# Kernel optimization log

Hardware: AMD Instinct MI355X
Metric: run time of the kernel (lower is better)

Reference implementation:

```python
import jax, jax.numpy as jnp
import numpy as np

# Mamba hyperparameters (match init_kwargs)
D_MODEL = 1024
D_STATE = 16
D_CONV = 4
EXPAND = 2
D_INNER = EXPAND * D_MODEL          # 2048
DT_RANK = D_MODEL // 16             # 64 (ceil(d_model/16))
B, L = 2, 2048
LN_EPS = 1e-5


def setup_inputs() -> dict:
    key = jax.random.key(0)
    ks = jax.random.split(key, 8)
    s = lambda k, shape, scale=0.02: jax.random.normal(k, shape, jnp.float32) * scale
    x = jax.random.normal(ks[0], (B, L, D_MODEL), jnp.float32)
    W_in = s(ks[1], (2 * D_INNER, D_MODEL))                 # in_proj (no bias)
    W_conv = s(ks[2], (D_INNER, 1, D_CONV), 0.1)            # depthwise conv1d weight
    b_conv = jnp.zeros((D_INNER,), jnp.float32)
    W_xproj = s(ks[3], (DT_RANK + 2 * D_STATE, D_INNER))    # x_proj (no bias)
    W_dt = s(ks[4], (D_INNER, DT_RANK), 0.1)                # dt_proj weight
    b_dt = s(ks[5], (D_INNER,), 0.5)                        # dt_proj bias
    # A initialized as -exp(A_log) with A_log = log(1..d_state), as in mamba_ssm
    A_log = jnp.log(jnp.broadcast_to(
        jnp.arange(1, D_STATE + 1, dtype=jnp.float32), (D_INNER, D_STATE)))
    D_skip = jnp.ones((D_INNER,), jnp.float32)
    W_out = s(ks[6], (D_MODEL, D_INNER))                    # out_proj (no bias)
    gamma = jnp.ones((D_MODEL,), jnp.float32)
    beta = jnp.zeros((D_MODEL,), jnp.float32)
    return dict(x=x, W_in=W_in, W_conv=W_conv, b_conv=b_conv, W_xproj=W_xproj,
                W_dt=W_dt, b_dt=b_dt, A_log=A_log, D_skip=D_skip, W_out=W_out,
                gamma=gamma, beta=beta)


def _mamba(x, W_in, W_conv, b_conv, W_xproj, W_dt, b_dt, A_log, D_skip, W_out):
    # in_proj -> split into x branch and gate z branch, each [B, L, d_inner]
    xz = jnp.einsum('bld,ed->ble', x, W_in)
    xin, z = jnp.split(xz, 2, axis=-1)

    # causal depthwise conv1d over time, then SiLU
    xc = jnp.swapaxes(xin, 1, 2)                            # [B, d_inner, L]
    xc = jnp.pad(xc, ((0, 0), (0, 0), (D_CONV - 1, 0)))
    xc = jax.lax.conv_general_dilated(
        xc, W_conv, window_strides=(1,), padding='VALID',
        dimension_numbers=('NCH', 'OIH', 'NCH'), feature_group_count=D_INNER)
    xc = xc + b_conv[None, :, None]
    u = jax.nn.silu(jnp.swapaxes(xc, 1, 2))                 # [B, L, d_inner]

    # input-dependent dt, B, C
    xdb = jnp.einsum('ble,fe->blf', u, W_xproj)
    dt, Bm, Cm = jnp.split(xdb, [DT_RANK, DT_RANK + D_STATE], axis=-1)
    delta = jax.nn.softplus(jnp.einsum('blr,er->ble', dt, W_dt) + b_dt)  # [B,L,E]
    A = -jnp.exp(A_log)                                     # [E, N]

    def step(h, inp):
        d_t, B_t, C_t, u_t = inp                            # [B,E],[B,N],[B,N],[B,E]
        dA = jnp.exp(d_t[..., None] * A)                    # [B, E, N]
        dBu = d_t[..., None] * B_t[:, None, :] * u_t[..., None]
        h = dA * h + dBu                                    # [B, E, N]
        y = jnp.einsum('ben,bn->be', h, C_t)
        return h, y

    h0 = jnp.zeros((B, D_INNER, D_STATE), x.dtype)
    xs = (jnp.swapaxes(delta, 0, 1), jnp.swapaxes(Bm, 0, 1),
          jnp.swapaxes(Cm, 0, 1), jnp.swapaxes(u, 0, 1))
    _, ys = jax.lax.scan(step, h0, xs)                      # ys: [L, B, E]
    y = jnp.swapaxes(ys, 0, 1) + u * D_skip
    y = y * jax.nn.silu(z)                                  # gated
    return jnp.einsum('ble,de->bld', y, W_out)


def reference(x, W_in, W_conv, b_conv, W_xproj, W_dt, b_dt, A_log, D_skip,
              W_out, gamma, beta):
    out = x + _mamba(x, W_in, W_conv, b_conv, W_xproj, W_dt, b_dt, A_log,
                     D_skip, W_out)
    mu = jnp.mean(out, axis=-1, keepdims=True)
    var = jnp.mean(jnp.square(out - mu), axis=-1, keepdims=True)
    return (out - mu) * jax.lax.rsqrt(var + LN_EPS) * gamma + beta
```

## Files before the change

### kernel.cpp

```cpp
#include <hip/hip_runtime.h>
#include <cstdint>
#include <cstddef>

#define D_MODEL   1024
#define D_STATE   16
#define D_CONV    4
#define D_INNER   2048
#define DT_RANK   64
#define NBATCH    2
#define SEQ       2048
#define NTOK      (NBATCH*SEQ)
#define LN_EPSF   1e-5f
#define NCHUNK    64
#define TCHUNK    32
#define KSPLIT    8

typedef unsigned short u16;
typedef __bf16 bf16x8 __attribute__((ext_vector_type(8)));
typedef float  f32x4  __attribute__((ext_vector_type(4)));

__device__ __forceinline__ u16 f2bf(float f) {
  unsigned u = __float_as_uint(f);
  u += 0x7fffu + ((u >> 16) & 1u);
  return (u16)(u >> 16);
}
__device__ __forceinline__ float bf2f(u16 v) {
  return __uint_as_float(((unsigned)v) << 16);
}
__device__ __forceinline__ void unpack8(uint4 v, float* f) {
  f[0] = __uint_as_float(v.x << 16); f[1] = __uint_as_float(v.x & 0xffff0000u);
  f[2] = __uint_as_float(v.y << 16); f[3] = __uint_as_float(v.y & 0xffff0000u);
  f[4] = __uint_as_float(v.z << 16); f[5] = __uint_as_float(v.z & 0xffff0000u);
  f[6] = __uint_as_float(v.w << 16); f[7] = __uint_as_float(v.w & 0xffff0000u);
}

__device__ __forceinline__ void async16(const u16* g, u16* l) {
  __builtin_amdgcn_global_load_lds(
      (const __attribute__((address_space(1))) unsigned*)g,
      (__attribute__((address_space(3))) unsigned*)l, 16, 0, 0);
}

#define PN0 (NTOK*D_MODEL)
#define PN1 (2*D_INNER*D_MODEL)
#define PN2 (128*D_INNER)
#define PN3 (D_INNER*DT_RANK)
#define PN4 (D_MODEL*D_INNER)
#define PTOT (PN0+PN1+PN2+PN3+PN4)
__global__ __launch_bounds__(256) void prep_k(
    const float* __restrict__ x, const float* __restrict__ W_in,
    const float* __restrict__ W_xproj, const float* __restrict__ W_dt,
    const float* __restrict__ W_out,
    u16* __restrict__ x_bf, u16* __restrict__ Win_bf, u16* __restrict__ Wxp_bf,
    u16* __restrict__ Wdt_bf, u16* __restrict__ Wout_bf)
{
  int i = (blockIdx.x * 256 + threadIdx.x) * 4;
  const float* src; u16* dst; bool pad = false; int local = i;
  if (local < PN0)            { src = x;       dst = x_bf; }
  else if ((local -= PN0) < PN1) { src = W_in;    dst = Win_bf; }
  else if ((local -= PN1) < PN2) { src = W_xproj; dst = Wxp_bf; pad = (local >> 11) >= 96; }
  else if ((local -= PN2) < PN3) { src = W_dt;    dst = Wdt_bf; }
  else if ((local -= PN3) < PN4) { src = W_out;   dst = Wout_bf; }
  else return;
  ushort4 o;
  if (pad) { o = (ushort4){0,0,0,0}; }
  else {
    const float4 v = *(const float4*)(src + local);
    o = (ushort4){ f2bf(v.x), f2bf(v.y), f2bf(v.z), f2bf(v.w) };
  }
  *(ushort4*)(dst + local) = o;
}

template<int BM, int BN, int KB, int WTM, int WTN, int EPI>
__global__ __launch_bounds__(256) void gemm_nt(
    const u16* __restrict__ A, const u16* __restrict__ B,
    float* __restrict__ C, u16* __restrict__ Cb,
    const float* __restrict__ bias, const float* __restrict__ res,
    int kStart, int kEnd, int lda, int ldb, int ldc, size_t partStride)
{
  constexpr int CPR  = KB / 8;
  constexpr int MASK = CPR - 1;
  constexpr int KSUB = KB / 32;
  constexpr int WAVES_N = BN / (16 * WTN);
  constexpr int ACH = BM * CPR;
  constexpr int BCH = BN * CPR;
  constexpr int ROUNDS = (ACH + BCH) / 256;

  __shared__ __align__(16) u16 lA[BM * KB];
  __shared__ __align__(16) u16 lB[BN * KB];

  const int tid  = threadIdx.x;
  const int w    = tid >> 6;
  const int lane = tid & 63;
  const int lrow = lane & 15;
  const int quad = lane >> 4;
  const int bm = blockIdx.y * BM;
  const int bn = blockIdx.x * BN;
  const int wave_m = (w / WAVES_N) * (16 * WTM);
  const int wave_n = (w % WAVES_N) * (16 * WTN);

  int kOff = 0;
  if constexpr (EPI == 4) kOff = blockIdx.z * (kEnd - kStart);

  f32x4 acc[WTM][WTN];
  #pragma unroll
  for (int mi = 0; mi < WTM; ++mi)
    #pragma unroll
    for (int ni = 0; ni < WTN; ++ni)
      acc[mi][ni] = (f32x4){0.f, 0.f, 0.f, 0.f};

  for (int k0 = kStart + kOff; k0 < kEnd + kOff; k0 += KB) {
    #pragma unroll
    for (int r = 0; r < ROUNDS; ++r) {
      const int c0 = r * 256 + w * 64;
      const int c  = c0 + lane;
      if (c0 < ACH) {
        const int row = c / CPR, cc = (c & MASK) ^ (row & MASK);
        async16(A + (size_t)(bm + row) * lda + k0 + cc * 8, &lA[c0 * 8]);
      } else {
        const int cb = c - ACH, c0b = c0 - ACH;
        const int row = cb / CPR, cc = (cb & MASK) ^ (row & MASK);
        async16(B + (size_t)(bn + row) * ldb + k0 + cc * 8, &lB[c0b * 8]);
      }
    }
    __syncthreads();

    #pragma unroll
    for (int s = 0; s < KSUB; ++s) {
      bf16x8 af[WTM], bfv[WTN];
      #pragma unroll
      for (int mi = 0; mi < WTM; ++mi) {
        const int R = wave_m + mi * 16 + lrow;
        af[mi] = *(const bf16x8*)&lA[R * KB + (((s * 4 + quad) ^ (R & MASK)) * 8)];
      }
      #pragma unroll
      for (int ni = 0; ni < WTN; ++ni) {
        const int R = wave_n + ni * 16 + lrow;
        bfv[ni] = *(const bf16x8*)&lB[R * KB + (((s * 4 + quad) ^ (R & MASK)) * 8)];
      }
      #pragma unroll
      for (int mi = 0; mi < WTM; ++mi)
        #pragma unroll
        for (int ni = 0; ni < WTN; ++ni)
          acc[mi][ni] = __builtin_amdgcn_mfma_f32_16x16x32_bf16(af[mi], bfv[ni], acc[mi][ni], 0, 0, 0);
    }
    __syncthreads();
  }

  #pragma unroll
  for (int mi = 0; mi < WTM; ++mi) {
    #pragma unroll
    for (int ni = 0; ni < WTN; ++ni) {
      const int col  = bn + wave_n + ni * 16 + lrow;
      const int row0 = bm + wave_m + mi * 16 + quad * 4;
      #pragma unroll
      for (int r = 0; r < 4; ++r) {
        float v = acc[mi][ni][r];
        const size_t idx = (size_t)(row0 + r) * ldc + col;
        if constexpr (EPI == 0) {
          C[idx] = v;
        } else if constexpr (EPI == 1) {
          Cb[idx] = f2bf(v);
        } else if constexpr (EPI == 2) {
          v += bias[col];
          v = (v > 20.f) ? v : log1pf(__expf(v));
          Cb[idx] = f2bf(v);
        } else if constexpr (EPI == 3) {
          C[idx] = v + res[idx];
        } else {
          C[(size_t)blockIdx.z * partStride + idx] = v;
        }
      }
    }
  }
}

__global__ __launch_bounds__(256) void reduce_conv_k(
    const float* __restrict__ part, u16* __restrict__ dst)
{
  const int i = blockIdx.x * 256 + threadIdx.x;
  float s = 0.f;
  #pragma unroll
  for (int p = 0; p < KSPLIT; ++p)
    s += part[(size_t)p * (NTOK * 128) + i];
  dst[i] = f2bf(s);
}

#define CONV_T 8
__global__ __launch_bounds__(256) void conv_silu_k(
    const u16* __restrict__ xz, const float* __restrict__ Wc,
    const float* __restrict__ bc, u16* __restrict__ ub)
{
  const int tid = blockIdx.x * 256 + threadIdx.x;
  const int e   = (tid & 511) * 4;
  const int tb  = tid >> 9;
  const int tok0 = tb * CONV_T;
  const int l0   = tok0 & (SEQ - 1);

  float4 wq[4];
  #pragma unroll
  for (int q = 0; q < 4; ++q) wq[q] = *(const float4*)(Wc + (e + q) * 4);
  const float4 bcv = *(const float4*)(bc + e);

  float p3[4], p2[4], p1[4];
  if (l0 == 0) {
    #pragma unroll
    for (int q = 0; q < 4; ++q) { p3[q] = 0.f; p2[q] = 0.f; p1[q] = 0.f; }
  } else {
    const ushort4 a = *(const ushort4*)(xz + (size_t)(tok0 - 3) * (2 * D_INNER) + e);
    const ushort4 b = *(const ushort4*)(xz + (size_t)(tok0 - 2) * (2 * D_INNER) + e);
    const ushort4 c = *(const ushort4*)(xz + (size_t)(tok0 - 1) * (2 * D_INNER) + e);
    p3[0]=bf2f(a.x); p3[1]=bf2f(a.y); p3[2]=bf2f(a.z); p3[3]=bf2f(a.w);
    p2[0]=bf2f(b.x); p2[1]=bf2f(b.y); p2[2]=bf2f(b.z); p2[3]=bf2f(b.w);
    p1[0]=bf2f(c.x); p1[1]=bf2f(c.y); p1[2]=bf2f(c.z); p1[3]=bf2f(c.w);
  }

  #pragma unroll
  for (int tt = 0; tt < CONV_T; ++tt) {
    const ushort4 xv = *(const ushort4*)(xz + (size_t)(tok0 + tt) * (2 * D_INNER) + e);
    float cur[4] = { bf2f(xv.x), bf2f(xv.y), bf2f(xv.z), bf2f(xv.w) };
    ushort4 o;
    u16* op = (u16*)&o;
    float a0 = ((const float*)&bcv)[0] + p3[0]*wq[0].x + p2[0]*wq[0].y + p1[0]*wq[0].z + cur[0]*wq[0].w;
    float a1 = ((const float*)&bcv)[1] + p3[1]*wq[1].x + p2[1]*wq[1].y + p1[1]*wq[1].z + cur[1]*wq[1].w;
    float a2 = ((const float*)&bcv)[2] + p3[2]*wq[2].x + p2[2]*wq[2].y + p1[2]*wq[2].z + cur[2]*wq[2].w;
    float a3 = ((const float*)&bcv)[3] + p3[3]*wq[3].x + p2[3]*wq[3].y + p1[3]*wq[3].z + cur[3]*wq[3].w;
    op[0] = f2bf(a0 / (1.f + __expf(-a0)));
    op[1] = f2bf(a1 / (1.f + __expf(-a1)));
    op[2] = f2bf(a2 / (1.f + __expf(-a2)));
    op[3] = f2bf(a3 / (1.f + __expf(-a3)));
    *(ushort4*)(ub + (size_t)(tok0 + tt) * D_INNER + e) = o;
    #pragma unroll
    for (int q = 0; q < 4; ++q) { p3[q] = p2[q]; p2[q] = p1[q]; p1[q] = cur[q]; }
  }
}


__global__ __launch_bounds__(256) void scan_p1(
    const u16* __restrict__ delta, const u16* __restrict__ ub,
    const u16* __restrict__ xdb, const float* __restrict__ A_log,
    float* __restrict__ S, float* __restrict__ sumd)
{
  const int e = blockIdx.x * 256 + threadIdx.x;
  const int c = blockIdx.y;
  const int b = blockIdx.z;
  float A[16], h[16];
  bool fast = true;
  #pragma unroll
  for (int n = 0; n < 16; ++n) {
    A[n] = -__expf(A_log[e * 16 + n]);
    fast = fast && (fabsf(A[n] + (float)(n + 1)) < 1e-3f);
    h[n] = 0.f;
  }
  float sd = 0.f;
  const int t0 = c * TCHUNK;
  #pragma unroll 2
  for (int t = 0; t < TCHUNK; ++t) {
    const size_t g = (size_t)(b * SEQ + t0 + t);
    const float dlt = bf2f(delta[g * D_INNER + e]);
    const float ut  = bf2f(ub[g * D_INNER + e]);
    float Bv[16];
    const u16* bp = xdb + g * 128 + DT_RANK;
    unpack8(*(const uint4*)bp, Bv);
    unpack8(*(const uint4*)(bp + 8), Bv + 8);
    sd += dlt;
    const float dbu = dlt * ut;
    float dA[16];
    if (fast) {
      const float q = __expf(-dlt);
      float p = 1.f;
      #pragma unroll
      for (int n = 0; n < 16; ++n) { p *= q; dA[n] = p; }
    } else {
      #pragma unroll
      for (int n = 0; n < 16; ++n) dA[n] = __expf(dlt * A[n]);
    }
    #pragma unroll
    for (int n = 0; n < 16; ++n)
      h[n] = dA[n] * h[n] + dbu * Bv[n];
  }
  const size_t idx = ((size_t)(b * NCHUNK + c) * D_INNER + e);
  #pragma unroll
  for (int q = 0; q < 4; ++q)
    *(f32x4*)&S[idx * 16 + q * 4] = (f32x4){h[q*4], h[q*4+1], h[q*4+2], h[q*4+3]};
  sumd[idx] = sd;
}

__global__ __launch_bounds__(256) void scan_p2(
    const float* __restrict__ S, const float* __restrict__ sumd,
    const float* __restrict__ A_log, float* __restrict__ hinit)
{
  const int tid = blockIdx.x * 256 + threadIdx.x;
  const int n = tid & 15;
  const int e = (tid >> 4) & (D_INNER - 1);
  const int b = tid >> 15;
  const float An = -__expf(A_log[e * 16 + n]);
  float h = 0.f;
  size_t idx = (size_t)b * NCHUNK * D_INNER + e;
  float s_cur  = S[idx * 16 + n];
  float sd_cur = sumd[idx];
  for (int c = 0; c < NCHUNK; ++c) {
    hinit[idx * 16 + n] = h;
    float s_nxt = 0.f, sd_nxt = 0.f;
    if (c + 1 < NCHUNK) {
      const size_t idx2 = idx + D_INNER;
      s_nxt  = S[idx2 * 16 + n];
      sd_nxt = sumd[idx2];
    }
    h = __expf(An * sd_cur) * h + s_cur;
    s_cur = s_nxt; sd_cur = sd_nxt;
    idx += D_INNER;
  }
}

__global__ __launch_bounds__(256) void scan_p3(
    const u16* __restrict__ delta, const u16* __restrict__ ub,
    const u16* __restrict__ xdb, const u16* __restrict__ xz,
    const float* __restrict__ A_log, const float* __restrict__ D_skip,
    const float* __restrict__ hinit, u16* __restrict__ yg)
{
  const int e = blockIdx.x * 256 + threadIdx.x;
  const int c = blockIdx.y;
  const int b = blockIdx.z;
  const size_t idx = ((size_t)(b * NCHUNK + c) * D_INNER + e);
  float A[16], h[16];
  bool fast = true;
  #pragma unroll
  for (int n = 0; n < 16; ++n) {
    A[n] = -__expf(A_log[e * 16 + n]);
    fast = fast && (fabsf(A[n] + (float)(n + 1)) < 1e-3f);
  }
  #pragma unroll
  for (int q = 0; q < 4; ++q) {
    f32x4 v = *(const f32x4*)&hinit[idx * 16 + q * 4];
    h[q*4] = v[0]; h[q*4+1] = v[1]; h[q*4+2] = v[2]; h[q*4+3] = v[3];
  }
  const float De = D_skip[e];
  const int t0 = c * TCHUNK;
  #pragma unroll 2
  for (int t = 0; t < TCHUNK; ++t) {
    const size_t g = (size_t)(b * SEQ + t0 + t);
    const float dlt = bf2f(delta[g * D_INNER + e]);
    const float ut  = bf2f(ub[g * D_INNER + e]);
    const float z   = bf2f(xz[g * (2 * D_INNER) + D_INNER + e]);
    float Bv[16], Cv[16];
    const u16* bp = xdb + g * 128 + DT_RANK;
    unpack8(*(const uint4*)bp, Bv);
    unpack8(*(const uint4*)(bp + 8), Bv + 8);
    unpack8(*(const uint4*)(bp + 16), Cv);
    unpack8(*(const uint4*)(bp + 24), Cv + 8);
    const float dbu = dlt * ut;
    float dA[16];
    if (fast) {
      const float q = __expf(-dlt);
      float p = 1.f;
      #pragma unroll
      for (int n = 0; n < 16; ++n) { p *= q; dA[n] = p; }
    } else {
      #pragma unroll
      for (int n = 0; n < 16; ++n) dA[n] = __expf(dlt * A[n]);
    }
    float y = 0.f;
    #pragma unroll
    for (int n = 0; n < 16; ++n) {
      h[n] = dA[n] * h[n] + dbu * Bv[n];
      y += h[n] * Cv[n];
    }
    y += ut * De;
    const float gt = z / (1.f + __expf(-z));
    yg[g * D_INNER + e] = f2bf(y * gt);
  }
}

__global__ __launch_bounds__(256) void ln_k(const float* __restrict__ pre,
                                            const float* __restrict__ gamma,
                                            const float* __restrict__ beta,
                                            float* __restrict__ out)
{
  const int tok = blockIdx.x;
  const int t   = threadIdx.x;
  const float* row = pre + (size_t)tok * D_MODEL;
  float v[4], s = 0.f, s2 = 0.f;
  #pragma unroll
  for (int i = 0; i < 4; ++i) {
    v[i] = row[t + i * 256];
    s += v[i]; s2 += v[i] * v[i];
  }
  #pragma unroll
  for (int off = 32; off >= 1; off >>= 1) {
    s  += __shfl_xor(s,  off);
    s2 += __shfl_xor(s2, off);
  }
  __shared__ float red[8];
  if ((t & 63) == 0) { red[t >> 6] = s; red[4 + (t >> 6)] = s2; }
  __syncthreads();
  if (t == 0) {
    const float ts  = red[0] + red[1] + red[2] + red[3];
    const float ts2 = red[4] + red[5] + red[6] + red[7];
    const float mu  = ts * (1.f / D_MODEL);
    const float var = ts2 * (1.f / D_MODEL) - mu * mu;
    red[0] = mu; red[1] = rsqrtf(var + LN_EPSF);
  }
  __syncthreads();
  const float mu = red[0], rv = red[1];
  #pragma unroll
  for (int i = 0; i < 4; ++i) {
    const int c = t + i * 256;
    out[(size_t)tok * D_MODEL + c] = (v[i] - mu) * rv * gamma[c] + beta[c];
  }
}

extern "C" void kernel_launch(void* const* d_in, const int* in_sizes, int n_in,
                              void* d_out, int out_size, void* d_ws, size_t ws_size,
                              hipStream_t stream) {
  const float* x       = (const float*)d_in[0];
  const float* W_in    = (const float*)d_in[1];
  const float* W_conv  = (const float*)d_in[2];
  const float* b_conv  = (const float*)d_in[3];
  const float* W_xproj = (const float*)d_in[4];
  const float* W_dt    = (const float*)d_in[5];
  const float* b_dt    = (const float*)d_in[6];
  const float* A_log   = (const float*)d_in[7];
  const float* D_skip  = (const float*)d_in[8];
  const float* W_out   = (const float*)d_in[9];
  const float* gamma   = (const float*)d_in[10];
  const float* beta    = (const float*)d_in[11];
  float* out = (float*)d_out;

  char* ws = (char*)d_ws;
  size_t used = 0;
  auto alloc = [&](size_t bytes) -> char* {
    char* p = ws + used;
    used += (bytes + 255) & ~(size_t)255;
    return p;
  };
  u16* xz_bf     = (u16*)alloc((size_t)NTOK * 2 * D_INNER * 2);
  float* pre     = (float*)alloc((size_t)NTOK * D_MODEL * 4);
  char*  xw_reg  = alloc((size_t)NTOK * D_MODEL * 2 + (size_t)2 * D_INNER * D_MODEL * 2);
  u16* u_bf      = (u16*)alloc((size_t)NTOK * D_INNER * 2);
  u16* delta_bf  = (u16*)alloc((size_t)NTOK * D_INNER * 2);
  u16* xdb_bf    = (u16*)alloc((size_t)NTOK * 128 * 2);
  u16* Wxp_bf    = (u16*)alloc((size_t)128 * D_INNER * 2);
  u16* Wdt_bf    = (u16*)alloc((size_t)D_INNER * DT_RANK * 2);
  u16* Wout_bf   = (u16*)alloc((size_t)D_MODEL * D_INNER * 2);
  u16* yg_bf     = (u16*)alloc((size_t)NTOK * D_INNER * 2);
  float* sumd    = (float*)alloc((size_t)NBATCH * NCHUNK * D_INNER * 4);
  float* xdb_part= (float*)alloc((size_t)KSPLIT * NTOK * 128 * 4);

  u16* x_bf    = (u16*)xw_reg;
  u16* Win_bf  = (u16*)(xw_reg + (size_t)NTOK * D_MODEL * 2);
  float* S     = pre;
  float* hinit = (float*)xw_reg;

  if (ws_size < used) {
    hipMemsetAsync(d_out, 0xFF, (size_t)out_size * 4, stream);
    return;
  }

  const dim3 blk(256);

  prep_k<<<(PTOT / 4 + 255) / 256, blk, 0, stream>>>(
      x, W_in, W_xproj, W_dt, W_out, x_bf, Win_bf, Wxp_bf, Wdt_bf, Wout_bf);

  gemm_nt<128,128,64,4,4,1><<<dim3((2*D_INNER)/128, NTOK/128), blk, 0, stream>>>(
      x_bf, Win_bf, nullptr, xz_bf, nullptr, nullptr,
      0, D_MODEL, D_MODEL, D_MODEL, 2*D_INNER, 0);

  conv_silu_k<<<(NTOK / CONV_T) * (D_INNER / 4) / 256, blk, 0, stream>>>(
      xz_bf, W_conv, b_conv, u_bf);

  gemm_nt<64,128,32,1,8,4><<<dim3(1, NTOK/64, KSPLIT), blk, 0, stream>>>(
      u_bf, Wxp_bf, xdb_part, nullptr, nullptr, nullptr,
      0, D_INNER / KSPLIT, D_INNER, D_INNER, 128, (size_t)NTOK * 128);
  reduce_conv_k<<<(NTOK * 128) / 256, blk, 0, stream>>>(xdb_part, xdb_bf);

  gemm_nt<128,128,64,4,4,2><<<dim3(D_INNER/128, NTOK/128), blk, 0, stream>>>(
      xdb_bf, Wdt_bf, nullptr, delta_bf, b_dt, nullptr,
      0, DT_RANK, 128, DT_RANK, D_INNER, 0);

  scan_p1<<<dim3(D_INNER/256, NCHUNK, NBATCH), blk, 0, stream>>>(
      delta_bf, u_bf, xdb_bf, A_log, S, sumd);
  scan_p2<<<(NBATCH * D_INNER * D_STATE) / 256, blk, 0, stream>>>(
      S, sumd, A_log, hinit);
  scan_p3<<<dim3(D_INNER/256, NCHUNK, NBATCH), blk, 0, stream>>>(
      delta_bf, u_bf, xdb_bf, xz_bf, A_log, D_skip, hinit, yg_bf);

  gemm_nt<128,64,64,4,2,3><<<dim3(D_MODEL/64, NTOK/128), blk, 0, stream>>>(
      yg_bf, Wout_bf, pre, nullptr, nullptr, x,
      0, D_INNER, D_INNER, D_INNER, D_MODEL, 0);

  ln_k<<<NTOK, blk, 0, stream>>>(pre, gamma, beta, out);
}
```

Before: 312.1 us.

## Split scan state buffers into per-quad planes and swap out_proj grid order

The chunk-state buffers S and hinit are stored as four planes of float4 (one per group of four states), so the scan_p1 and scan_p3 vector stores and loads become contiguous across threads. scan_p2 is remapped so each wave handles one plane and lanes read adjacent addresses, instead of strided 64-byte rows. The out_proj GEMM also swaps its grid axes so consecutive blocks walk along M, which changes the L2 reuse pattern for the W_out tiles. These changes aim to fix uncoalesced scan state traffic and improve cache locality, at the cost of a more complex indexing scheme.

```diff
diff --git a/kernel.cpp b/kernel.cpp
--- a/kernel.cpp
+++ b/kernel.cpp
@@ -70,7 +70,7 @@
   *(ushort4*)(dst + local) = o;
 }
 
-template<int BM, int BN, int KB, int WTM, int WTN, int EPI>
+template<int BM, int BN, int KB, int WTM, int WTN, int EPI, int SWAPG>
 __global__ __launch_bounds__(256) void gemm_nt(
     const u16* __restrict__ A, const u16* __restrict__ B,
     float* __restrict__ C, u16* __restrict__ Cb,
@@ -93,8 +93,8 @@
   const int lane = tid & 63;
   const int lrow = lane & 15;
   const int quad = lane >> 4;
-  const int bm = blockIdx.y * BM;
-  const int bn = blockIdx.x * BN;
+  const int bm = (SWAPG ? blockIdx.x : blockIdx.y) * BM;
+  const int bn = (SWAPG ? blockIdx.y : blockIdx.x) * BN;
   const int wave_m = (w / WAVES_N) * (16 * WTM);
   const int wave_n = (w % WAVES_N) * (16 * WTN);
 
@@ -234,6 +234,7 @@
   }
 }
 
+#define SPLANE (D_INNER * 4)
 
 __global__ __launch_bounds__(256) void scan_p1(
     const u16* __restrict__ delta, const u16* __restrict__ ub,
@@ -278,37 +279,40 @@
     for (int n = 0; n < 16; ++n)
       h[n] = dA[n] * h[n] + dbu * Bv[n];
   }
-  const size_t idx = ((size_t)(b * NCHUNK + c) * D_INNER + e);
+  const size_t sbase = ((size_t)(b * NCHUNK + c) * 4) * SPLANE + e * 4;
   #pragma unroll
   for (int q = 0; q < 4; ++q)
-    *(f32x4*)&S[idx * 16 + q * 4] = (f32x4){h[q*4], h[q*4+1], h[q*4+2], h[q*4+3]};
-  sumd[idx] = sd;
+    *(f32x4*)&S[sbase + (size_t)q * SPLANE] = (f32x4){h[q*4], h[q*4+1], h[q*4+2], h[q*4+3]};
+  sumd[(size_t)(b * NCHUNK + c) * D_INNER + e] = sd;
 }
 
 __global__ __launch_bounds__(256) void scan_p2(
     const float* __restrict__ S, const float* __restrict__ sumd,
     const float* __restrict__ A_log, float* __restrict__ hinit)
 {
-  const int tid = blockIdx.x * 256 + threadIdx.x;
-  const int n = tid & 15;
-  const int e = (tid >> 4) & (D_INNER - 1);
-  const int b = tid >> 15;
+  const int q    = threadIdx.x >> 6;
+  const int lane = threadIdx.x & 63;
+  const int e    = blockIdx.x * 16 + (lane >> 2);
+  const int r    = lane & 3;
+  const int b    = blockIdx.y;
+  const int n    = q * 4 + r;
   const float An = -__expf(A_log[e * 16 + n]);
   float h = 0.f;
-  size_t idx = (size_t)b * NCHUNK * D_INNER + e;
-  float s_cur  = S[idx * 16 + n];
-  float sd_cur = sumd[idx];
+  size_t sidx = ((size_t)(b * NCHUNK) * 4 + q) * SPLANE + e * 4 + r;
+  size_t didx = (size_t)(b * NCHUNK) * D_INNER + e;
+  float s_cur  = S[sidx];
+  float sd_cur = sumd[didx];
   for (int c = 0; c < NCHUNK; ++c) {
-    hinit[idx * 16 + n] = h;
+    hinit[sidx] = h;
     float s_nxt = 0.f, sd_nxt = 0.f;
     if (c + 1 < NCHUNK) {
-      const size_t idx2 = idx + D_INNER;
-      s_nxt  = S[idx2 * 16 + n];
-      sd_nxt = sumd[idx2];
+      s_nxt  = S[sidx + 4 * SPLANE];
+      sd_nxt = sumd[didx + D_INNER];
     }
     h = __expf(An * sd_cur) * h + s_cur;
     s_cur = s_nxt; sd_cur = sd_nxt;
-    idx += D_INNER;
+    sidx += 4 * SPLANE;
+    didx += D_INNER;
   }
 }
 
@@ -321,7 +325,6 @@
   const int e = blockIdx.x * 256 + threadIdx.x;
   const int c = blockIdx.y;
   const int b = blockIdx.z;
-  const size_t idx = ((size_t)(b * NCHUNK + c) * D_INNER + e);
   float A[16], h[16];
   bool fast = true;
   #pragma unroll
@@ -329,9 +332,10 @@
     A[n] = -__expf(A_log[e * 16 + n]);
     fast = fast && (fabsf(A[n] + (float)(n + 1)) < 1e-3f);
   }
+  const size_t sbase = ((size_t)(b * NCHUNK + c) * 4) * SPLANE + e * 4;
   #pragma unroll
   for (int q = 0; q < 4; ++q) {
-    f32x4 v = *(const f32x4*)&hinit[idx * 16 + q * 4];
+    f32x4 v = *(const f32x4*)&hinit[sbase + (size_t)q * SPLANE];
     h[q*4] = v[0]; h[q*4+1] = v[1]; h[q*4+2] = v[2]; h[q*4+3] = v[3];
   }
   const float De = D_skip[e];
@@ -461,30 +465,30 @@
   prep_k<<<(PTOT / 4 + 255) / 256, blk, 0, stream>>>(
       x, W_in, W_xproj, W_dt, W_out, x_bf, Win_bf, Wxp_bf, Wdt_bf, Wout_bf);
 
-  gemm_nt<128,128,64,4,4,1><<<dim3((2*D_INNER)/128, NTOK/128), blk, 0, stream>>>(
+  gemm_nt<128,128,64,4,4,1,0><<<dim3((2*D_INNER)/128, NTOK/128), blk, 0, stream>>>(
       x_bf, Win_bf, nullptr, xz_bf, nullptr, nullptr,
       0, D_MODEL, D_MODEL, D_MODEL, 2*D_INNER, 0);
 
   conv_silu_k<<<(NTOK / CONV_T) * (D_INNER / 4) / 256, blk, 0, stream>>>(
       xz_bf, W_conv, b_conv, u_bf);
 
-  gemm_nt<64,128,32,1,8,4><<<dim3(1, NTOK/64, KSPLIT), blk, 0, stream>>>(
+  gemm_nt<64,128,32,1,8,4,0><<<dim3(1, NTOK/64, KSPLIT), blk, 0, stream>>>(
       u_bf, Wxp_bf, xdb_part, nullptr, nullptr, nullptr,
       0, D_INNER / KSPLIT, D_INNER, D_INNER, 128, (size_t)NTOK * 128);
   reduce_conv_k<<<(NTOK * 128) / 256, blk, 0, stream>>>(xdb_part, xdb_bf);
 
-  gemm_nt<128,128,64,4,4,2><<<dim3(D_INNER/128, NTOK/128), blk, 0, stream>>>(
+  gemm_nt<128,128,64,4,4,2,0><<<dim3(D_INNER/128, NTOK/128), blk, 0, stream>>>(
       xdb_bf, Wdt_bf, nullptr, delta_bf, b_dt, nullptr,
       0, DT_RANK, 128, DT_RANK, D_INNER, 0);
 
   scan_p1<<<dim3(D_INNER/256, NCHUNK, NBATCH), blk, 0, stream>>>(
       delta_bf, u_bf, xdb_bf, A_log, S, sumd);
-  scan_p2<<<(NBATCH * D_INNER * D_STATE) / 256, blk, 0, stream>>>(
+  scan_p2<<<dim3(D_INNER/16, NBATCH), blk, 0, stream>>>(
       S, sumd, A_log, hinit);
   scan_p3<<<dim3(D_INNER/256, NCHUNK, NBATCH), blk, 0, stream>>>(
       delta_bf, u_bf, xdb_bf, xz_bf, A_log, D_skip, hinit, yg_bf);
 
-  gemm_nt<128,64,64,4,2,3><<<dim3(D_MODEL/64, NTOK/128), blk, 0, stream>>>(
+  gemm_nt<128,64,64,4,2,3,1><<<dim3(NTOK/128, D_MODEL/64), blk, 0, stream>>>(
       yg_bf, Wout_bf, pre, nullptr, nullptr, x,
       0, D_INNER, D_INNER, D_INNER, D_MODEL, 0);
 
```

Result: no change. 309.7 us (-0.8%).
